# Optimization experiments

Hardware: AMD Instinct MI355X
Metric: run time of the kernel (lower is better)

## Reference

```python
import jax, jax.numpy as jnp
import numpy as np

B, N, C = 8, 1024, 1024
H = 16
D = C // H  # head_dim = 64


def apply_rope(t, cos, sin):
    # t: (B,H,N,D), cos/sin: (N, D//2). Interleaved-pair RoPE
    # (matches repeat_interleave(2) + stack(-y2,y1) in the torch code).
    tr = t.reshape(*t.shape[:-1], D // 2, 2)
    t1, t2 = tr[..., 0], tr[..., 1]
    o1 = t1 * cos - t2 * sin
    o2 = t2 * cos + t1 * sin
    return jnp.stack((o1, o2), axis=-1).reshape(t.shape)


def setup_inputs() -> dict:
    key = jax.random.key(0)
    k1, k2, k3, k4 = jax.random.split(key, 4)
    s = 0.02
    x = jax.random.normal(k1, (B, N, C), dtype=jnp.float32)
    w_qkv = jax.random.normal(k2, (C, 3 * C), dtype=jnp.float32) * s  # qkv_bias=False
    w_proj = jax.random.normal(k3, (C, C), dtype=jnp.float32) * s
    b_proj = jax.random.normal(k4, (C,), dtype=jnp.float32) * s
    return {"x": x, "w_qkv": w_qkv, "w_proj": w_proj, "b_proj": b_proj}


def reference(x, w_qkv, w_proj, b_proj):
    # QKV projection: (B,N,3C) -> (3,B,H,N,D)
    qkv = (x @ w_qkv).reshape(B, N, 3, H, D).transpose(2, 0, 3, 1, 4)
    q, k, v = qkv[0], qkv[1], qkv[2]

    # RoPE tables: pos = arange(N) (mask=None, no cls/registers)
    pos = jnp.arange(N, dtype=jnp.float32)
    omega = 1.0 / (10000.0 ** (jnp.arange(D // 2, dtype=jnp.float32) / (D / 2.0)))
    freq = pos[:, None] * omega  # (N, D//2)
    cos, sin = jnp.cos(freq), jnp.sin(freq)

    q = apply_rope(q, cos, sin)
    k = apply_rope(k, cos, sin)

    # Scaled dot-product attention (non-causal, no dropout in eval)
    scale = 1.0 / jnp.sqrt(jnp.float32(D))
    scores = jnp.einsum('bhqd,bhkd->bhqk', q, k) * scale
    attn = jax.nn.softmax(scores, axis=-1)
    out = jnp.einsum('bhqk,bhkd->bhqd', attn, v)

    # Merge heads + output projection
    out = out.transpose(0, 2, 1, 3).reshape(B, N, C)
    return out @ w_proj + b_proj
```

## Files before the change

### kernel.cpp

```cpp
#include <hip/hip_runtime.h>
#include <hip/hip_bf16.h>
#include <math.h>

#define Bsz  8
#define Nseq 1024
#define Cdim 1024
#define Hh   16
#define Dd   64

typedef short short8 __attribute__((ext_vector_type(8)));
typedef float floatx4 __attribute__((ext_vector_type(4)));

__device__ __forceinline__ unsigned short f2bf(float f) {
    __hip_bfloat16 h = __float2bfloat16(f);
    return __builtin_bit_cast(unsigned short, h);
}

__device__ __forceinline__ void async16(const void* g, void* l) {
    __builtin_amdgcn_global_load_lds(
        (const __attribute__((address_space(1))) unsigned int*)g,
        (__attribute__((address_space(3))) unsigned int*)l, 16, 0, 0);
}

__device__ __forceinline__ unsigned pack_bf16(float lo, float hi) {
    unsigned ulo = __float_as_uint(lo) + 0x8000u;
    unsigned uhi = __float_as_uint(hi) + 0x8000u;
    return __builtin_amdgcn_perm(uhi, ulo, 0x07060302);
}

__global__ __launch_bounds__(256) void prep(
    const float* __restrict__ x, const float* __restrict__ w_qkv,
    const float* __restrict__ w_proj,
    unsigned short* __restrict__ xb, unsigned short* __restrict__ wqkvt,
    unsigned short* __restrict__ wprojt, float2* __restrict__ rope)
{
    __shared__ float T[64][65];
    const int blk = blockIdx.x;
    const int tid = threadIdx.x;

    if (blk < 8192) {
        int i = blk * 256 + tid;
        float4 v = ((const float4*)x)[i];
        ushort4 u;
        u.x = f2bf(v.x); u.y = f2bf(v.y); u.z = f2bf(v.z); u.w = f2bf(v.w);
        ((ushort4*)xb)[i] = u;
        return;
    }
    if (blk < 9216) {
        const float* in;
        unsigned short* out;
        int R = 1024, Ccols, c0, r0;
        if (blk < 8960) {
            int b2 = blk - 8192;
            in = w_qkv; out = wqkvt; Ccols = 3072;
            c0 = (b2 % 48) * 64; r0 = (b2 / 48) * 64;
        } else {
            int b2 = blk - 8960;
            in = w_proj; out = wprojt; Ccols = 1024;
            c0 = (b2 % 16) * 64; r0 = (b2 / 16) * 64;
        }
        for (int i = tid; i < 4096; i += 256) {
            int r = i >> 6, c = i & 63;
            T[r][c] = in[(size_t)(r0 + r) * Ccols + c0 + c];
        }
        __syncthreads();
        for (int i = tid; i < 4096; i += 256) {
            int rr = i >> 6, cc = i & 63;
            out[(size_t)(c0 + rr) * R + r0 + cc] = f2bf(T[cc][rr]);
        }
        return;
    }
    {
        int i = (blk - 9216) * 256 + tid;
        int n = i >> 5, p = i & 31;
        float omega = __expf(-(float)p * 0.2878231366242557f);
        float sv, cv;
        sincosf((float)n * omega, &sv, &cv);
        rope[i] = make_float2(cv, sv);
    }
}

template <int MODE>
__global__ __launch_bounds__(256) void gemm_bf16(
    const unsigned short* __restrict__ A, const unsigned short* __restrict__ Bt,
    const float* __restrict__ bias, const float2* __restrict__ rope,
    unsigned short* __restrict__ qb, unsigned short* __restrict__ kb,
    unsigned short* __restrict__ vtb, float* __restrict__ out)
{
    const int K = 1024;
    __shared__ short SM[2][128][64];
    const int tid  = threadIdx.x;
    const int wave = tid >> 6, lane = tid & 63;
    const int ml = lane & 15, quad = lane >> 4;
    const int wm = wave >> 1, wn = wave & 1;

    int lin = blockIdx.y * gridDim.x + blockIdx.x;
    const int nwg = gridDim.x * gridDim.y;
    lin = (lin & 7) * (nwg >> 3) + (lin >> 3);
    const int bx = lin % gridDim.x, by = lin / gridDim.x;
    const int bm = by * 128, bn = bx * 128;

    const int lr     = lane >> 3;
    const int lchunk = ((lane & 7) ^ lr) * 8;

    floatx4 acc[4][4] = {};

    for (int k0 = 0; k0 < K; k0 += 64) {
        #pragma unroll
        for (int t = 0; t < 4; ++t) {
            int r8  = (wave * 4 + t) * 8;
            int row = r8 + lr;
            async16(A  + (size_t)(bm + row) * K + k0 + lchunk, &SM[0][r8][0]);
            async16(Bt + (size_t)(bn + row) * K + k0 + lchunk, &SM[1][r8][0]);
        }
        __syncthreads();

        #pragma unroll
        for (int ks = 0; ks < 2; ++ks) {
            const int sl = ((ks * 4 + quad) ^ (ml & 7)) * 8;
            short8 araw[4], braw[4];
            #pragma unroll
            for (int mi = 0; mi < 4; ++mi)
                araw[mi] = *(const short8*)&SM[0][wm * 64 + mi * 16 + ml][sl];
            #pragma unroll
            for (int ni = 0; ni < 4; ++ni)
                braw[ni] = *(const short8*)&SM[1][wn * 64 + ni * 16 + ml][sl];
            #pragma unroll
            for (int mi = 0; mi < 4; ++mi)
                #pragma unroll
                for (int ni = 0; ni < 4; ++ni)
                    acc[mi][ni] = __builtin_amdgcn_mfma_f32_16x16x32_bf16(
                        araw[mi], braw[ni], acc[mi][ni], 0, 0, 0);
        }
        __syncthreads();
    }

    if (MODE == 0) {
        const int region = bn >> 10;
        const int b = bm >> 10;
        if (region < 2) {
            float2* Rs = (float2*)&SM[0][0][0];
            #pragma unroll
            for (int t = 0; t < 16; ++t) {
                int idx = t * 256 + tid;
                Rs[idx] = rope[(size_t)((bm + (idx >> 5)) & 1023) * 32 + (idx & 31)];
            }
            __syncthreads();
            unsigned short* dst = (region == 0) ? qb : kb;
            const float scale = (region == 0) ? 0.125f : 1.f;
            const float sgn = (ml & 1) ? 1.f : -1.f;
            #pragma unroll
            for (int ni = 0; ni < 4; ++ni) {
                int col = bn + wn * 64 + ni * 16 + ml;
                int jj = col & 1023;
                int h = jj >> 6, d = jj & 63;
                int p = d >> 1;
                #pragma unroll
                for (int mi = 0; mi < 4; ++mi)
                    #pragma unroll
                    for (int r = 0; r < 4; ++r) {
                        int rl = wm * 64 + mi * 16 + quad * 4 + r;
                        int n  = (bm + rl) & 1023;
                        float val = acc[mi][ni][r];
                        float partner = __shfl_xor(val, 1);
                        float2 cs = Rs[rl * 32 + p];
                        dst[(((size_t)(b * Hh + h)) * Nseq + n) * Dd + d] =
                            f2bf((val * cs.x + sgn * partner * cs.y) * scale);
                    }
            }
        } else {
            short* T = &SM[0][0][0];
            const int n0 = bm & 1023;
            #pragma unroll
            for (int hw = 0; hw < 2; ++hw) {
                if (hw) __syncthreads();
                if (wn == hw) {
                    #pragma unroll
                    for (int ni = 0; ni < 4; ++ni) {
                        int dcol = ni * 16 + ml;
                        #pragma unroll
                        for (int mi = 0; mi < 4; ++mi)
                            #pragma unroll
                            for (int r = 0; r < 4; ++r) {
                                int rl = wm * 64 + mi * 16 + quad * 4 + r;
                                T[dcol * 132 + rl] = (short)f2bf(acc[mi][ni][r]);
                            }
                    }
                }
                __syncthreads();
                int h = ((bn & 1023) >> 6) + hw;
                #pragma unroll
                for (int t = 0; t < 8; ++t) {
                    int idx4 = t * 256 + tid;
                    int d = idx4 >> 5, seg = idx4 & 31;
                    ushort4 v4 = *(const ushort4*)&T[d * 132 + seg * 4];
                    *(ushort4*)(vtb + (((size_t)(b * Hh + h)) * Dd + d) * Nseq
                                + n0 + seg * 4) = v4;
                }
            }
        }
    } else {
        #pragma unroll
        for (int ni = 0; ni < 4; ++ni) {
            int col = bn + wn * 64 + ni * 16 + ml;
            float bv = bias[col];
            #pragma unroll
            for (int mi = 0; mi < 4; ++mi)
                #pragma unroll
                for (int r = 0; r < 4; ++r) {
                    int row = bm + wm * 64 + mi * 16 + quad * 4 + r;
                    out[(size_t)row * 1024 + col] = acc[mi][ni][r] + bv;
                }
        }
    }
}

__global__ __launch_bounds__(256, 3) void attn_flash_mfma(
    const unsigned short* __restrict__ qb, const unsigned short* __restrict__ kb,
    const unsigned short* __restrict__ vt, unsigned short* __restrict__ ao)
{
    const int bh  = blockIdx.x;
    const int qt  = blockIdx.y;
    const int tid = threadIdx.x;
    const int wave = tid >> 6, lane = tid & 63;
    const int ml = lane & 15, quad = lane >> 4;
    const int lr = lane >> 3;
    const int lc = ((lane & 7) ^ lr) * 8;

    __shared__ __attribute__((aligned(16))) short SMEM[25600];
    short* const KsB = SMEM;
    short* const VsB = SMEM + 8192;
    short (*Qs)[64] = (short(*)[64])(SMEM + 16384);
    short* const PsB = SMEM + 16384;
    const int psw = 16384 + wave * 2304;

    const size_t hbase = (size_t)bh * (Nseq * Dd);
    const size_t vbase = (size_t)bh * 64;
    const int q0 = qt * 128;
    const int wq = wave * 32;
    const int wk = wave * 16;
    (void)PsB;

    #pragma unroll
    for (int t = 0; t < 4; ++t)
        async16(qb + hbase + (size_t)(q0 + wq + t * 8 + lr) * 64 + lc, &Qs[wq + t * 8][0]);
    async16(kb + hbase + (size_t)(wk + lr) * 64 + lc,     KsB + (wk)     * 64);
    async16(kb + hbase + (size_t)(wk + 8 + lr) * 64 + lc, KsB + (wk + 8) * 64);
    async16(vt + (vbase + wk + lr) * Nseq + lc,           VsB + (wk)     * 64);
    async16(vt + (vbase + wk + 8 + lr) * Nseq + lc,       VsB + (wk + 8) * 64);
    __syncthreads();

    short8 qfr[2][2];
    #pragma unroll
    for (int ks = 0; ks < 2; ++ks) {
        const int sl = ((ks * 4 + quad) ^ (ml & 7)) * 8;
        qfr[ks][0] = *(const short8*)&Qs[wq + ml][sl];
        qfr[ks][1] = *(const short8*)&Qs[wq + 16 + ml][sl];
    }
    __syncthreads();

    float l0 = 0.f, l1 = 0.f;
    floatx4 o[2][4] = {};

    for (int kt = 0; kt < 16; ++kt) {
        const int bu = kt & 1;
        const short* Kb = KsB + bu * 4096;
        const short* Vb = VsB + bu * 4096;

        if (kt < 15) {
            const int k1r = (kt + 1) * 64;
            short* Kn = KsB + (bu ^ 1) * 4096;
            short* Vn = VsB + (bu ^ 1) * 4096;
            async16(kb + hbase + (size_t)(k1r + wk + lr) * 64 + lc,     Kn + (wk)     * 64);
            async16(kb + hbase + (size_t)(k1r + wk + 8 + lr) * 64 + lc, Kn + (wk + 8) * 64);
            async16(vt + (vbase + wk + lr) * Nseq + k1r + lc,           Vn + (wk)     * 64);
            async16(vt + (vbase + wk + 8 + lr) * Nseq + k1r + lc,       Vn + (wk + 8) * 64);
        }

        floatx4 st[2][4] = {};
        __builtin_amdgcn_s_setprio(1);
        #pragma unroll
        for (int ks = 0; ks < 2; ++ks) {
            const int sl = ((ks * 4 + quad) ^ (ml & 7)) * 8;
            #pragma unroll
            for (int kbk = 0; kbk < 4; ++kbk) {
                short8 kf = *(const short8*)&Kb[(kbk * 16 + ml) * 64 + sl];
                st[0][kbk] = __builtin_amdgcn_mfma_f32_16x16x32_bf16(kf, qfr[ks][0], st[0][kbk], 0, 0, 0);
                st[1][kbk] = __builtin_amdgcn_mfma_f32_16x16x32_bf16(kf, qfr[ks][1], st[1][kbk], 0, 0, 0);
            }
        }
        __builtin_amdgcn_s_setprio(0);

        #pragma unroll
        for (int qg = 0; qg < 2; ++qg) {
            float lacc = 0.f;
            #pragma unroll
            for (int kbk = 0; kbk < 4; ++kbk) {
                float e0 = __expf(st[qg][kbk][0]);
                float e1 = __expf(st[qg][kbk][1]);
                float e2 = __expf(st[qg][kbk][2]);
                float e3 = __expf(st[qg][kbk][3]);
                lacc += (e0 + e1) + (e2 + e3);
                uint2 pk;
                pk.x = pack_bf16(e0, e1);
                pk.y = pack_bf16(e2, e3);
                *(uint2*)&SMEM[psw + (qg * 16 + ml) * 72 + kbk * 16 + quad * 4] = pk;
            }
            if (qg == 0) l0 += lacc; else l1 += lacc;
        }
        asm volatile("s_waitcnt lgkmcnt(0)" ::: "memory");
        __builtin_amdgcn_sched_barrier(0);

        __builtin_amdgcn_s_setprio(1);
        #pragma unroll
        for (int ks = 0; ks < 2; ++ks) {
            const int sl = ((ks * 4 + quad) ^ (ml & 7)) * 8;
            short8 pf0 = *(const short8*)&SMEM[psw + (ml) * 72 + ks * 32 + quad * 8];
            short8 pf1 = *(const short8*)&SMEM[psw + (16 + ml) * 72 + ks * 32 + quad * 8];
            #pragma unroll
            for (int nt = 0; nt < 4; ++nt) {
                short8 vf = *(const short8*)&Vb[(nt * 16 + ml) * 64 + sl];
                o[0][nt] = __builtin_amdgcn_mfma_f32_16x16x32_bf16(pf0, vf, o[0][nt], 0, 0, 0);
                o[1][nt] = __builtin_amdgcn_mfma_f32_16x16x32_bf16(pf1, vf, o[1][nt], 0, 0, 0);
            }
        }
        __builtin_amdgcn_s_setprio(0);

        if (kt < 15) {
            asm volatile("s_waitcnt vmcnt(0)" ::: "memory");
            __builtin_amdgcn_s_barrier();
        }
    }

    l0 += __shfl_xor(l0, 16);
    l0 += __shfl_xor(l0, 32);
    l1 += __shfl_xor(l1, 16);
    l1 += __shfl_xor(l1, 32);

    const int b = bh >> 4, h = bh & 15;
    #pragma unroll
    for (int qg = 0; qg < 2; ++qg) {
        float lsrc = (qg == 0) ? l0 : l1;
        #pragma unroll
        for (int r = 0; r < 4; ++r) {
            float lq = __shfl(lsrc, quad * 4 + r);
            float inv = 1.f / lq;
            int q = q0 + wq + qg * 16 + quad * 4 + r;
            size_t rowbase = ((size_t)(b * Nseq + q)) * Cdim + h * Dd;
            #pragma unroll
            for (int nt = 0; nt < 4; ++nt)
                ao[rowbase + nt * 16 + ml] = f2bf(o[qg][nt][r] * inv);
        }
    }
}

extern "C" void kernel_launch(void* const* d_in, const int* in_sizes, int n_in,
                              void* d_out, int out_size, void* d_ws, size_t ws_size,
                              hipStream_t stream) {
    const float* x      = (const float*)d_in[0];
    const float* w_qkv  = (const float*)d_in[1];
    const float* w_proj = (const float*)d_in[2];
    const float* b_proj = (const float*)d_in[3];
    float* out = (float*)d_out;

    const size_t M8 = (size_t)8 * 1024 * 1024;
    unsigned short* qb     = (unsigned short*)d_ws;
    unsigned short* kb     = qb + M8;
    unsigned short* vt     = kb + M8;
    unsigned short* xb     = vt + M8;
    unsigned short* wqkvt  = xb + M8;
    unsigned short* wprojt = wqkvt + 3 * 1024 * 1024;
    float2*         rope   = (float2*)(wprojt + 1024 * 1024);
    unsigned short* aob    = xb;

    prep<<<9344, 256, 0, stream>>>(x, w_qkv, w_proj, xb, wqkvt, wprojt, rope);

    gemm_bf16<0><<<dim3(24, 64), 256, 0, stream>>>(xb, wqkvt, nullptr, rope,
                                                   qb, kb, vt, nullptr);

    attn_flash_mfma<<<dim3(128, 8), 256, 0, stream>>>(qb, kb, vt, aob);

    gemm_bf16<1><<<dim3(8, 64), 256, 0, stream>>>(aob, wprojt, b_proj, nullptr,
                                                  nullptr, nullptr, nullptr, out);
}
```

Baseline: 239.8 us.

## Pass softmax probabilities via lane shuffles instead of LDS and raise occupancy

The attention kernel no longer stages the P tile in shared memory. Exponentiated scores are packed into registers and redistributed into the MFMA A-operand layout with cross-lane shuffles, which drops the per-wave P buffer and shrinks LDS from 50 KB to 32 KB per block, so launch bounds go from 3 to 4 blocks per CU. The log2(e) factor is folded into the Q scale so a raw v_exp_f32 (exp2) can replace __expf. The cost is many ds_bpermute shuffles per tile and more register pressure, which the higher occupancy target may turn into spills.

```diff
diff --git a/kernel.cpp b/kernel.cpp
--- a/kernel.cpp
+++ b/kernel.cpp
@@ -26,6 +26,12 @@
     unsigned ulo = __float_as_uint(lo) + 0x8000u;
     unsigned uhi = __float_as_uint(hi) + 0x8000u;
     return __builtin_amdgcn_perm(uhi, ulo, 0x07060302);
+}
+
+__device__ __forceinline__ float exp2_raw(float x) {
+    float r;
+    asm("v_exp_f32 %0, %1" : "=v"(r) : "v"(x));
+    return r;
 }
 
 __global__ __launch_bounds__(256) void prep(
@@ -147,7 +153,7 @@
             }
             __syncthreads();
             unsigned short* dst = (region == 0) ? qb : kb;
-            const float scale = (region == 0) ? 0.125f : 1.f;
+            const float scale = (region == 0) ? 0.1803368801111602f : 1.f;
             const float sgn = (ml & 1) ? 1.f : -1.f;
             #pragma unroll
             for (int ni = 0; ni < 4; ++ni) {
@@ -215,7 +221,7 @@
     }
 }
 
-__global__ __launch_bounds__(256, 3) void attn_flash_mfma(
+__global__ __launch_bounds__(256, 4) void attn_flash_mfma(
     const unsigned short* __restrict__ qb, const unsigned short* __restrict__ kb,
     const unsigned short* __restrict__ vt, unsigned short* __restrict__ ao)
 {
@@ -227,27 +233,22 @@
     const int lr = lane >> 3;
     const int lc = ((lane & 7) ^ lr) * 8;
 
-    __shared__ __attribute__((aligned(16))) short SMEM[25600];
-    short* const KsB = SMEM;
-    short* const VsB = SMEM + 8192;
-    short (*Qs)[64] = (short(*)[64])(SMEM + 16384);
-    short* const PsB = SMEM + 16384;
-    const int psw = 16384 + wave * 2304;
+    __shared__ __attribute__((aligned(16))) short SMEM[16384];
+    short (*Qs)[64] = (short(*)[64])(SMEM + 8192);
 
     const size_t hbase = (size_t)bh * (Nseq * Dd);
     const size_t vbase = (size_t)bh * 64;
     const int q0 = qt * 128;
     const int wq = wave * 32;
     const int wk = wave * 16;
-    (void)PsB;
 
     #pragma unroll
     for (int t = 0; t < 4; ++t)
         async16(qb + hbase + (size_t)(q0 + wq + t * 8 + lr) * 64 + lc, &Qs[wq + t * 8][0]);
-    async16(kb + hbase + (size_t)(wk + lr) * 64 + lc,     KsB + (wk)     * 64);
-    async16(kb + hbase + (size_t)(wk + 8 + lr) * 64 + lc, KsB + (wk + 8) * 64);
-    async16(vt + (vbase + wk + lr) * Nseq + lc,           VsB + (wk)     * 64);
-    async16(vt + (vbase + wk + 8 + lr) * Nseq + lc,       VsB + (wk + 8) * 64);
+    async16(kb + hbase + (size_t)(wk + lr) * 64 + lc,     SMEM + (wk) * 64);
+    async16(kb + hbase + (size_t)(wk + 8 + lr) * 64 + lc, SMEM + (wk + 8) * 64);
+    async16(vt + (vbase + wk + lr) * Nseq + lc,           SMEM + 4096 + (wk) * 64);
+    async16(vt + (vbase + wk + 8 + lr) * Nseq + lc,       SMEM + 4096 + (wk + 8) * 64);
     __syncthreads();
 
     short8 qfr[2][2];
@@ -261,20 +262,20 @@
 
     float l0 = 0.f, l1 = 0.f;
     floatx4 o[2][4] = {};
+    const int srcA = ml + ((quad & 1) << 5);
+    const int srcB = srcA + 16;
 
     for (int kt = 0; kt < 16; ++kt) {
-        const int bu = kt & 1;
-        const short* Kb = KsB + bu * 4096;
-        const short* Vb = VsB + bu * 4096;
+        const short* Kb = SMEM + (kt & 1) * 8192;
+        const short* Vb = Kb + 4096;
 
         if (kt < 15) {
+            short* Nb = SMEM + ((kt & 1) ^ 1) * 8192;
             const int k1r = (kt + 1) * 64;
-            short* Kn = KsB + (bu ^ 1) * 4096;
-            short* Vn = VsB + (bu ^ 1) * 4096;
-            async16(kb + hbase + (size_t)(k1r + wk + lr) * 64 + lc,     Kn + (wk)     * 64);
-            async16(kb + hbase + (size_t)(k1r + wk + 8 + lr) * 64 + lc, Kn + (wk + 8) * 64);
-            async16(vt + (vbase + wk + lr) * Nseq + k1r + lc,           Vn + (wk)     * 64);
-            async16(vt + (vbase + wk + 8 + lr) * Nseq + k1r + lc,       Vn + (wk + 8) * 64);
+            async16(kb + hbase + (size_t)(k1r + wk + lr) * 64 + lc,     Nb + (wk) * 64);
+            async16(kb + hbase + (size_t)(k1r + wk + 8 + lr) * 64 + lc, Nb + (wk + 8) * 64);
+            async16(vt + (vbase + wk + lr) * Nseq + k1r + lc,           Nb + 4096 + (wk) * 64);
+            async16(vt + (vbase + wk + 8 + lr) * Nseq + k1r + lc,       Nb + 4096 + (wk + 8) * 64);
         }
 
         floatx4 st[2][4] = {};
@@ -291,37 +292,51 @@
         }
         __builtin_amdgcn_s_setprio(0);
 
+        uint2 pk[2][4];
         #pragma unroll
         for (int qg = 0; qg < 2; ++qg) {
             float lacc = 0.f;
             #pragma unroll
             for (int kbk = 0; kbk < 4; ++kbk) {
-                float e0 = __expf(st[qg][kbk][0]);
-                float e1 = __expf(st[qg][kbk][1]);
-                float e2 = __expf(st[qg][kbk][2]);
-                float e3 = __expf(st[qg][kbk][3]);
+                float e0 = exp2_raw(st[qg][kbk][0]);
+                float e1 = exp2_raw(st[qg][kbk][1]);
+                float e2 = exp2_raw(st[qg][kbk][2]);
+                float e3 = exp2_raw(st[qg][kbk][3]);
                 lacc += (e0 + e1) + (e2 + e3);
-                uint2 pk;
-                pk.x = pack_bf16(e0, e1);
-                pk.y = pack_bf16(e2, e3);
-                *(uint2*)&SMEM[psw + (qg * 16 + ml) * 72 + kbk * 16 + quad * 4] = pk;
+                pk[qg][kbk].x = pack_bf16(e0, e1);
+                pk[qg][kbk].y = pack_bf16(e2, e3);
             }
             if (qg == 0) l0 += lacc; else l1 += lacc;
         }
-        asm volatile("s_waitcnt lgkmcnt(0)" ::: "memory");
-        __builtin_amdgcn_sched_barrier(0);
 
         __builtin_amdgcn_s_setprio(1);
         #pragma unroll
         for (int ks = 0; ks < 2; ++ks) {
             const int sl = ((ks * 4 + quad) ^ (ml & 7)) * 8;
-            short8 pf0 = *(const short8*)&SMEM[psw + (ml) * 72 + ks * 32 + quad * 8];
-            short8 pf1 = *(const short8*)&SMEM[psw + (16 + ml) * 72 + ks * 32 + quad * 8];
+            short8 pf[2];
+            #pragma unroll
+            for (int qg = 0; qg < 2; ++qg) {
+                int alx = __shfl((int)pk[qg][2 * ks].x,     srcA);
+                int aly = __shfl((int)pk[qg][2 * ks].y,     srcA);
+                int ahx = __shfl((int)pk[qg][2 * ks + 1].x, srcA);
+                int ahy = __shfl((int)pk[qg][2 * ks + 1].y, srcA);
+                int blx = __shfl((int)pk[qg][2 * ks].x,     srcB);
+                int bly = __shfl((int)pk[qg][2 * ks].y,     srcB);
+                int bhx = __shfl((int)pk[qg][2 * ks + 1].x, srcB);
+                int bhy = __shfl((int)pk[qg][2 * ks + 1].y, srcB);
+                const bool up = (quad >> 1) != 0;
+                int4 dv;
+                dv.x = up ? ahx : alx;
+                dv.y = up ? ahy : aly;
+                dv.z = up ? bhx : blx;
+                dv.w = up ? bhy : bly;
+                pf[qg] = __builtin_bit_cast(short8, dv);
+            }
             #pragma unroll
             for (int nt = 0; nt < 4; ++nt) {
                 short8 vf = *(const short8*)&Vb[(nt * 16 + ml) * 64 + sl];
-                o[0][nt] = __builtin_amdgcn_mfma_f32_16x16x32_bf16(pf0, vf, o[0][nt], 0, 0, 0);
-                o[1][nt] = __builtin_amdgcn_mfma_f32_16x16x32_bf16(pf1, vf, o[1][nt], 0, 0, 0);
+                o[0][nt] = __builtin_amdgcn_mfma_f32_16x16x32_bf16(pf[0], vf, o[0][nt], 0, 0, 0);
+                o[1][nt] = __builtin_amdgcn_mfma_f32_16x16x32_bf16(pf[1], vf, o[1][nt], 0, 0, 0);
             }
         }
         __builtin_amdgcn_s_setprio(0);
```

Result: no change. 243.3 us (+1.5%).
